# Kernel tuning notes

Measured on AMD Instinct MI355X. Metric: run time of the kernel, lower is better.

The kernel has to match this reference:

```python
import jax, jax.numpy as jnp
import numpy as np

B, T, C, HS = 32, 2048, 1024, 64

def setup_inputs() -> dict:
    key = jax.random.key(0)
    k1, k2, k3, k4 = jax.random.split(key, 4)
    x = jax.random.normal(k1, (B, T, C), dtype=jnp.float32)
    Wk = jax.random.normal(k2, (C, HS), dtype=jnp.float32) * (C ** -0.5)
    Wq = jax.random.normal(k3, (C, HS), dtype=jnp.float32) * (C ** -0.5)
    Wv = jax.random.normal(k4, (C, HS), dtype=jnp.float32) * (C ** -0.5)
    return {"x": x, "Wk": Wk, "Wq": Wq, "Wv": Wv}

def reference(x, Wk, Wq, Wv):
    # x: [B,T,C]; bias-free projections
    k = jnp.einsum('btc,ch->bth', x, Wk)   # [B,T,HS]
    q = jnp.einsum('btc,ch->bth', x, Wq)   # [B,T,HS]
    v = jnp.einsum('btc,ch->bth', x, Wv)   # [B,T,HS]
    Tdim = x.shape[1]
    Cdim = x.shape[2]
    scale = jax.lax.rsqrt(jnp.float32(Cdim))  # NOTE: source scales by rsqrt(C), not head_size
    wei = jnp.einsum('bth,bsh->bts', q, k) * scale  # [B,T,T]
    causal = jnp.tril(jnp.ones((Tdim, Tdim), dtype=bool))
    wei = jnp.where(causal, wei, -jnp.inf)
    wei = jax.nn.softmax(wei, axis=-1)
    out = jnp.einsum('bts,bsh->bth', wei, v)  # [B,T,HS]
    return out
```

## Files before the change

kernel.cpp:

```cpp
#include <hip/hip_runtime.h>
#include <hip/hip_bf16.h>

#define Bn 32
#define Tn 2048
#define Cn 1024
#define HSn 64

typedef __attribute__((ext_vector_type(8))) short short8;
typedef __attribute__((ext_vector_type(4))) float floatx4;

#if __has_builtin(__builtin_amdgcn_exp2f)
#define EXP2F __builtin_amdgcn_exp2f
#else
#define EXP2F exp2f
#endif

static __device__ __forceinline__ short f2bf(float f) {
    union { float f; unsigned u; } v; v.f = f;
    unsigned r = v.u + 0x7FFFu + ((v.u >> 16) & 1u);
    return (short)(r >> 16);
}
static __device__ __forceinline__ short f2bf_fast(float f) {
    union { float f; unsigned u; } v; v.f = f;
    return (short)((v.u + 0x8000u) >> 16);
}

static __device__ __forceinline__ void async16(const void* g, void* l) {
    __builtin_amdgcn_global_load_lds((const __attribute__((address_space(1))) void*)g,
                                     (__attribute__((address_space(3))) void*)l,
                                     16, 0, 0);
}

__global__ __launch_bounds__(256) void swz_w(const float* __restrict__ Wk,
                                             const float* __restrict__ Wq,
                                             const float* __restrict__ Wv,
                                             short* __restrict__ wswz) {
    int e = blockIdx.x * 256 + threadIdx.x;
    int j    = e & 7;
    int lane = (e >> 3) & 63;
    int grp  = e >> 9;
    int nt   = grp % 12;
    int kc   = grp / 12;
    int q = lane >> 4, m = lane & 15;
    int k = kc * 32 + q * 8 + j;
    int n = nt * 16 + m;
    const float* W = (n < 64) ? Wq : ((n < 128) ? Wk : Wv);
    wswz[e] = f2bf(W[k * 64 + (n & 63)]);
}

__global__ __launch_bounds__(256, 2) void qkv_gemm(const float* __restrict__ x,
                                                   const short* __restrict__ wswz,
                                                   short* __restrict__ qb,
                                                   short* __restrict__ kb,
                                                   short* __restrict__ vt) {
    __shared__ __align__(16) char lds[2][28 * 1024];

    int tid = threadIdx.x;
    int w = tid >> 6, l = tid & 63;
    int quad = l >> 4, m = l & 15;
    int r0 = blockIdx.x * 128;

    floatx4 acc[2][12];
#pragma unroll
    for (int r = 0; r < 2; r++)
#pragma unroll
        for (int nt = 0; nt < 12; nt++) acc[r][nt] = (floatx4)(0.0f);

    auto stage = [&](int kc, int bsel) {
        char* ab = &lds[bsel][0];
        char* bb = &lds[bsel][16 * 1024];
#pragma unroll
        for (int i = 0; i < 2; i++) {
            int rt = 2 * w + i;
            const float* src = x + (size_t)(r0 + rt * 16 + m) * Cn + kc * 32 + quad * 8;
            async16(src,     ab + rt * 2048 + l * 16);
            async16(src + 4, ab + rt * 2048 + 1024 + l * 16);
        }
#pragma unroll
        for (int i = 0; i < 3; i++) {
            int nt = 3 * w + i;
            const short* src = wswz + ((size_t)(kc * 12 + nt) * 64 + l) * 8;
            async16(src, bb + nt * 1024 + l * 16);
        }
    };

    stage(0, 0);
    for (int kc = 0; kc < 32; kc++) {
        __syncthreads();
        if (kc < 31) stage(kc + 1, (kc + 1) & 1);

        const char* ab = &lds[kc & 1][0];
        const char* bb = &lds[kc & 1][16 * 1024];

        short8 af[2];
#pragma unroll
        for (int r = 0; r < 2; r++) {
            int rt = 2 * w + r;
            float4 a0 = *(const float4*)(ab + rt * 2048 + l * 16);
            float4 a1 = *(const float4*)(ab + rt * 2048 + 1024 + l * 16);
            short8 t;
            t[0] = f2bf(a0.x); t[1] = f2bf(a0.y); t[2] = f2bf(a0.z); t[3] = f2bf(a0.w);
            t[4] = f2bf(a1.x); t[5] = f2bf(a1.y); t[6] = f2bf(a1.z); t[7] = f2bf(a1.w);
            af[r] = t;
        }
#pragma unroll
        for (int nt = 0; nt < 12; nt++) {
            short8 bf = *(const short8*)(bb + nt * 1024 + l * 16);
            acc[0][nt] = __builtin_amdgcn_mfma_f32_16x16x32_bf16(af[0], bf, acc[0][nt], 0, 0, 0);
            acc[1][nt] = __builtin_amdgcn_mfma_f32_16x16x32_bf16(af[1], bf, acc[1][nt], 0, 0, 0);
        }
    }

#pragma unroll
    for (int r = 0; r < 2; r++) {
        int rt = 2 * w + r;
#pragma unroll
        for (int reg = 0; reg < 4; reg++) {
            int g = r0 + rt * 16 + quad * 4 + reg;
            int b = g >> 11, t = g & (Tn - 1);
#pragma unroll
            for (int nt = 0; nt < 4; nt++)
                qb[(size_t)g * HSn + nt * 16 + m] = f2bf(acc[r][nt][reg]);
#pragma unroll
            for (int nt = 0; nt < 4; nt++)
                kb[(size_t)g * HSn + nt * 16 + m] = f2bf(acc[r][4 + nt][reg]);
#pragma unroll
            for (int nt = 0; nt < 4; nt++)
                vt[((size_t)b * HSn + nt * 16 + m) * Tn + t] = f2bf(acc[r][8 + nt][reg]);
        }
    }
}

__global__ __launch_bounds__(256, 4) void attn(const short* __restrict__ qb,
                                               const short* __restrict__ kb,
                                               const short* __restrict__ vt,
                                               float* __restrict__ out) {
    __shared__ __align__(16) short p_lds[4][16][72];
    __shared__ __align__(16) float comb[2][64][20];

    int tid = threadIdx.x;
    int w = tid >> 6, l = tid & 63;
    int quad = l >> 4, m = l & 15;
    int b  = blockIdx.x >> 5;
    int pb = blockIdx.x & 31;
    int pairSlot = w >> 1;
    int parity   = w & 1;
    int pairIdx  = pb * 2 + pairSlot;

    const short* kbbase = kb + (size_t)b * Tn * HSn;
    const short* vtbase = vt + (size_t)b * HSn * Tn;
    const float sl2e = 0.045084220027780106f;

    for (int half = 0; half < 2; half++) {
        int c = half ? (127 - pairIdx) : pairIdx;
        int r0 = c * 16;
        int jmax = c >> 2;

        size_t qoff = ((size_t)b * Tn + r0 + m) * HSn;
        short8 qf0 = *(const short8*)(qb + qoff + quad * 8);
        short8 qf1 = *(const short8*)(qb + qoff + 32 + quad * 8);

        floatx4 o[4];
#pragma unroll
        for (int i = 0; i < 4; i++) o[i] = (floatx4)(0.0f);
        float ps[4] = {0.f, 0.f, 0.f, 0.f};

        for (int j = parity; j <= jmax; j += 2) {
            floatx4 s[4];
#pragma unroll
            for (int i = 0; i < 4; i++) s[i] = (floatx4)(0.0f);
            const short* kt = kbbase + (size_t)j * 64 * HSn;
#pragma unroll
            for (int kc = 0; kc < 2; kc++) {
                short8 aq = kc ? qf1 : qf0;
#pragma unroll
                for (int nt = 0; nt < 4; nt++) {
                    short8 bk = *(const short8*)(kt + (size_t)(nt * 16 + m) * HSn + kc * 32 + quad * 8);
                    s[nt] = __builtin_amdgcn_mfma_f32_16x16x32_bf16(aq, bk, s[nt], 0, 0, 0);
                }
            }

            const short* vj = vtbase + j * 64;
            short8 bv[2][4];
#pragma unroll
            for (int kc = 0; kc < 2; kc++)
#pragma unroll
                for (int nt = 0; nt < 4; nt++)
                    bv[kc][nt] = *(const short8*)(vj + (size_t)(nt * 16 + m) * Tn + kc * 32 + quad * 8);

            if (j == jmax) {
                int rbase = r0 + quad * 4;
#pragma unroll
                for (int nt = 0; nt < 4; nt++)
#pragma unroll
                    for (int reg = 0; reg < 4; reg++) {
                        float p = EXP2F(s[nt][reg] * sl2e);
                        p = (j * 64 + nt * 16 + m > rbase + reg) ? 0.0f : p;
                        s[nt][reg] = p;
                        ps[reg] += p;
                    }
            } else {
#pragma unroll
                for (int nt = 0; nt < 4; nt++)
#pragma unroll
                    for (int reg = 0; reg < 4; reg++) {
                        float p = EXP2F(s[nt][reg] * sl2e);
                        s[nt][reg] = p;
                        ps[reg] += p;
                    }
            }

            asm volatile("" ::: "memory");
#pragma unroll
            for (int nt = 0; nt < 4; nt++)
#pragma unroll
                for (int reg = 0; reg < 4; reg++)
                    p_lds[w][quad * 4 + reg][nt * 16 + m] = f2bf_fast(s[nt][reg]);
            asm volatile("" ::: "memory");
            short8 ap0 = *(const short8*)(&p_lds[w][m][quad * 8]);
            short8 ap1 = *(const short8*)(&p_lds[w][m][32 + quad * 8]);

#pragma unroll
            for (int nt = 0; nt < 4; nt++)
                o[nt] = __builtin_amdgcn_mfma_f32_16x16x32_bf16(ap0, bv[0][nt], o[nt], 0, 0, 0);
#pragma unroll
            for (int nt = 0; nt < 4; nt++)
                o[nt] = __builtin_amdgcn_mfma_f32_16x16x32_bf16(ap1, bv[1][nt], o[nt], 0, 0, 0);
        }

        if (parity == 1) {
#pragma unroll
            for (int nt = 0; nt < 4; nt++)
                *(floatx4*)&comb[pairSlot][l][nt * 4] = o[nt];
            floatx4 pv; pv[0] = ps[0]; pv[1] = ps[1]; pv[2] = ps[2]; pv[3] = ps[3];
            *(floatx4*)&comb[pairSlot][l][16] = pv;
        }
        __syncthreads();
        if (parity == 0) {
#pragma unroll
            for (int nt = 0; nt < 4; nt++) {
                floatx4 t = *(const floatx4*)&comb[pairSlot][l][nt * 4];
                o[nt] += t;
            }
            floatx4 tp = *(const floatx4*)&comb[pairSlot][l][16];
            ps[0] += tp[0]; ps[1] += tp[1]; ps[2] += tp[2]; ps[3] += tp[3];
#pragma unroll
            for (int off = 1; off < 16; off <<= 1)
#pragma unroll
                for (int reg = 0; reg < 4; reg++)
                    ps[reg] += __shfl_xor(ps[reg], off, 64);
#pragma unroll
            for (int reg = 0; reg < 4; reg++) {
                float inv = 1.0f / ps[reg];
                int g = r0 + quad * 4 + reg;
#pragma unroll
                for (int nt = 0; nt < 4; nt++)
                    out[((size_t)b * Tn + g) * HSn + nt * 16 + m] = o[nt][reg] * inv;
            }
        }
        __syncthreads();
    }
}

extern "C" void kernel_launch(void* const* d_in, const int* in_sizes, int n_in,
                              void* d_out, int out_size, void* d_ws, size_t ws_size,
                              hipStream_t stream) {
    const float* x  = (const float*)d_in[0];
    const float* Wk = (const float*)d_in[1];
    const float* Wq = (const float*)d_in[2];
    const float* Wv = (const float*)d_in[3];
    float* out = (float*)d_out;

    char* ws = (char*)d_ws;
    short* wswz = (short*)ws;
    short* qb   = (short*)(ws + (1 << 19));
    short* kb   = (short*)(ws + (1 << 19) + (8 << 20));
    short* vt   = (short*)(ws + (1 << 19) + (16 << 20));

    swz_w<<<dim3(768), dim3(256), 0, stream>>>(Wk, Wq, Wv, wswz);
    qkv_gemm<<<dim3(512), dim3(256), 0, stream>>>(x, wswz, qb, kb, vt);
    attn<<<dim3(Bn * 32), dim3(256), 0, stream>>>(qb, kb, vt, out);
}
```

Before: 524.3 us.

## Stage K/V tiles in swizzled LDS shared by all four waves of attention block

The attention kernel now has each block handle one 64-row query tile per phase, with each wave owning 16 rows. K and V tiles are double-buffered into XOR-swizzled LDS with async copies, so the four waves share one load per tile instead of each reading from global memory. This drops the parity split and the LDS combine step, halves the grid to 512 blocks and lowers the occupancy hint to 2. The QKV GEMM staging pattern for x is also rearranged so each row's global reads are more contiguous. The risks are added barrier cost per tile and fewer blocks in flight.

New measurement: 449.8 us. -14.2%, faster.

```diff
diff --git a/kernel.cpp b/kernel.cpp
--- a/kernel.cpp
+++ b/kernel.cpp
@@ -69,12 +69,15 @@
     auto stage = [&](int kc, int bsel) {
         char* ab = &lds[bsel][0];
         char* bb = &lds[bsel][16 * 1024];
+        int srow = l & 15, sc = l >> 4;
 #pragma unroll
         for (int i = 0; i < 2; i++) {
             int rt = 2 * w + i;
-            const float* src = x + (size_t)(r0 + rt * 16 + m) * Cn + kc * 32 + quad * 8;
-            async16(src,     ab + rt * 2048 + l * 16);
-            async16(src + 4, ab + rt * 2048 + 1024 + l * 16);
+            const float* rbase = x + (size_t)(r0 + rt * 16 + srow) * Cn + kc * 32;
+#pragma unroll
+            for (int h = 0; h < 2; h++)
+                async16(rbase + h * 16 + sc * 4,
+                        ab + rt * 2048 + h * 1024 + l * 16);
         }
 #pragma unroll
         for (int i = 0; i < 3; i++) {
@@ -84,6 +87,8 @@
         }
     };
 
+    int c0 = (quad & 1) * 2, hh = quad >> 1;
+
     stage(0, 0);
     for (int kc = 0; kc < 32; kc++) {
         __syncthreads();
@@ -96,8 +101,9 @@
 #pragma unroll
         for (int r = 0; r < 2; r++) {
             int rt = 2 * w + r;
-            float4 a0 = *(const float4*)(ab + rt * 2048 + l * 16);
-            float4 a1 = *(const float4*)(ab + rt * 2048 + 1024 + l * 16);
+            const char* ap = ab + rt * 2048 + hh * 1024 + (c0 * 16 + m) * 16;
+            float4 a0 = *(const float4*)(ap);
+            float4 a1 = *(const float4*)(ap + 256);
             short8 t;
             t[0] = f2bf(a0.x); t[1] = f2bf(a0.y); t[2] = f2bf(a0.z); t[3] = f2bf(a0.w);
             t[4] = f2bf(a1.x); t[5] = f2bf(a1.y); t[6] = f2bf(a1.z); t[7] = f2bf(a1.w);
@@ -131,30 +137,41 @@
     }
 }
 
-__global__ __launch_bounds__(256, 4) void attn(const short* __restrict__ qb,
+__global__ __launch_bounds__(256, 2) void attn(const short* __restrict__ qb,
                                                const short* __restrict__ kb,
                                                const short* __restrict__ vt,
                                                float* __restrict__ out) {
+    __shared__ __align__(16) short kbuf[2][64 * 64];
+    __shared__ __align__(16) short vbuf[2][64 * 64];
     __shared__ __align__(16) short p_lds[4][16][72];
-    __shared__ __align__(16) float comb[2][64][20];
 
     int tid = threadIdx.x;
     int w = tid >> 6, l = tid & 63;
     int quad = l >> 4, m = l & 15;
-    int b  = blockIdx.x >> 5;
-    int pb = blockIdx.x & 31;
-    int pairSlot = w >> 1;
-    int parity   = w & 1;
-    int pairIdx  = pb * 2 + pairSlot;
+    int b = blockIdx.x >> 4;
+    int p = blockIdx.x & 15;
 
     const short* kbbase = kb + (size_t)b * Tn * HSn;
     const short* vtbase = vt + (size_t)b * HSn * Tn;
     const float sl2e = 0.045084220027780106f;
 
-    for (int half = 0; half < 2; half++) {
-        int c = half ? (127 - pairIdx) : pairIdx;
-        int r0 = c * 16;
-        int jmax = c >> 2;
+    int srow8 = l >> 3;
+    int schunk = l & 7;
+    auto stageKV = [&](int j, int s) {
+#pragma unroll
+        for (int i = 0; i < 2; i++) {
+            int r = w * 16 + i * 8 + srow8;
+            int c = schunk ^ (r & 7);
+            async16(kbbase + ((size_t)(j * 64 + r)) * HSn + c * 8,
+                    (char*)&kbuf[s][(w * 16 + i * 8) * 64] + l * 16);
+            async16(vtbase + (size_t)r * Tn + j * 64 + c * 8,
+                    (char*)&vbuf[s][(w * 16 + i * 8) * 64] + l * 16);
+        }
+    };
+
+    for (int phase = 0; phase < 2; phase++) {
+        int qt = phase ? (31 - p) : p;
+        int r0 = qt * 64 + w * 16;
 
         size_t qoff = ((size_t)b * Tn + r0 + m) * HSn;
         short8 qf0 = *(const short8*)(qb + qoff + quad * 8);
@@ -165,48 +182,48 @@
         for (int i = 0; i < 4; i++) o[i] = (floatx4)(0.0f);
         float ps[4] = {0.f, 0.f, 0.f, 0.f};
 
-        for (int j = parity; j <= jmax; j += 2) {
+        stageKV(0, 0);
+        for (int j = 0; j <= qt; j++) {
+            __syncthreads();
+            if (j < qt) stageKV(j + 1, (j + 1) & 1);
+
+            const short* kt = &kbuf[j & 1][0];
+            const short* vv = &vbuf[j & 1][0];
+            int swz = m & 7;
+
             floatx4 s[4];
 #pragma unroll
             for (int i = 0; i < 4; i++) s[i] = (floatx4)(0.0f);
-            const short* kt = kbbase + (size_t)j * 64 * HSn;
 #pragma unroll
             for (int kc = 0; kc < 2; kc++) {
                 short8 aq = kc ? qf1 : qf0;
 #pragma unroll
                 for (int nt = 0; nt < 4; nt++) {
-                    short8 bk = *(const short8*)(kt + (size_t)(nt * 16 + m) * HSn + kc * 32 + quad * 8);
+                    short8 bk = *(const short8*)(kt + (nt * 16 + m) * 64 +
+                                                 ((kc * 4 + quad) ^ swz) * 8);
                     s[nt] = __builtin_amdgcn_mfma_f32_16x16x32_bf16(aq, bk, s[nt], 0, 0, 0);
                 }
             }
 
-            const short* vj = vtbase + j * 64;
-            short8 bv[2][4];
-#pragma unroll
-            for (int kc = 0; kc < 2; kc++)
+            if (j == qt) {
+                int rloc = w * 16 + quad * 4;
 #pragma unroll
                 for (int nt = 0; nt < 4; nt++)
-                    bv[kc][nt] = *(const short8*)(vj + (size_t)(nt * 16 + m) * Tn + kc * 32 + quad * 8);
-
-            if (j == jmax) {
-                int rbase = r0 + quad * 4;
-#pragma unroll
-                for (int nt = 0; nt < 4; nt++)
 #pragma unroll
                     for (int reg = 0; reg < 4; reg++) {
-                        float p = EXP2F(s[nt][reg] * sl2e);
-                        p = (j * 64 + nt * 16 + m > rbase + reg) ? 0.0f : p;
-                        s[nt][reg] = p;
-                        ps[reg] += p;
+                        float pv = EXP2F(s[nt][reg] * sl2e);
+                        pv = (nt * 16 + m > rloc + reg) ? 0.0f : pv;
+                        s[nt][reg] = pv;
+                        ps[reg] += pv;
                     }
             } else {
 #pragma unroll
                 for (int nt = 0; nt < 4; nt++)
 #pragma unroll
                     for (int reg = 0; reg < 4; reg++) {
-                        float p = EXP2F(s[nt][reg] * sl2e);
-                        s[nt][reg] = p;
-                        ps[reg] += p;
+                        float pv = EXP2F(s[nt][reg] * sl2e);
+                        s[nt][reg] = pv;
+                        ps[reg] += pv;
                     }
             }
 
@@ -221,44 +238,31 @@
             short8 ap1 = *(const short8*)(&p_lds[w][m][32 + quad * 8]);
 
 #pragma unroll
-            for (int nt = 0; nt < 4; nt++)
-                o[nt] = __builtin_amdgcn_mfma_f32_16x16x32_bf16(ap0, bv[0][nt], o[nt], 0, 0, 0);
-#pragma unroll
-            for (int nt = 0; nt < 4; nt++)
-                o[nt] = __builtin_amdgcn_mfma_f32_16x16x32_bf16(ap1, bv[1][nt], o[nt], 0, 0, 0);
-        }
-
-        if (parity == 1) {
-#pragma unroll
-            for (int nt = 0; nt < 4; nt++)
-                *(floatx4*)&comb[pairSlot][l][nt * 4] = o[nt];
-            floatx4 pv; pv[0] = ps[0]; pv[1] = ps[1]; pv[2] = ps[2]; pv[3] = ps[3];
-            *(floatx4*)&comb[pairSlot][l][16] = pv;
+            for (int nt = 0; nt < 4; nt++) {
+                short8 bv0 = *(const short8*)(vv + (nt * 16 + m) * 64 + ((0 + quad) ^ swz) * 8);
+                o[nt] = __builtin_amdgcn_mfma_f32_16x16x32_bf16(ap0, bv0, o[nt], 0, 0, 0);
+            }
+#pragma unroll
+            for (int nt = 0; nt < 4; nt++) {
+                short8 bv1 = *(const short8*)(vv + (nt * 16 + m) * 64 + ((4 + quad) ^ swz) * 8);
+                o[nt] = __builtin_amdgcn_mfma_f32_16x16x32_bf16(ap1, bv1, o[nt], 0, 0, 0);
+            }
         }
         __syncthreads();
-        if (parity == 0) {
-#pragma unroll
-            for (int nt = 0; nt < 4; nt++) {
-                floatx4 t = *(const floatx4*)&comb[pairSlot][l][nt * 4];
-                o[nt] += t;
-            }
-            floatx4 tp = *(const floatx4*)&comb[pairSlot][l][16];
-            ps[0] += tp[0]; ps[1] += tp[1]; ps[2] += tp[2]; ps[3] += tp[3];
-#pragma unroll
-            for (int off = 1; off < 16; off <<= 1)
-#pragma unroll
-                for (int reg = 0; reg < 4; reg++)
-                    ps[reg] += __shfl_xor(ps[reg], off, 64);
-#pragma unroll
-            for (int reg = 0; reg < 4; reg++) {
-                float inv = 1.0f / ps[reg];
-                int g = r0 + quad * 4 + reg;
-#pragma unroll
-                for (int nt = 0; nt < 4; nt++)
-                    out[((size_t)b * Tn + g) * HSn + nt * 16 + m] = o[nt][reg] * inv;
-            }
-        }
-        __syncthreads();
+
+#pragma unroll
+        for (int off = 1; off < 16; off <<= 1)
+#pragma unroll
+            for (int reg = 0; reg < 4; reg++)
+                ps[reg] += __shfl_xor(ps[reg], off, 64);
+#pragma unroll
+        for (int reg = 0; reg < 4; reg++) {
+            float inv = 1.0f / ps[reg];
+            int g = r0 + quad * 4 + reg;
+#pragma unroll
+            for (int nt = 0; nt < 4; nt++)
+                out[((size_t)b * Tn + g) * HSn + nt * 16 + m] = o[nt][reg] * inv;
+        }
     }
 }
 
@@ -279,5 +283,5 @@
 
     swz_w<<<dim3(768), dim3(256), 0, stream>>>(Wk, Wq, Wv, wswz);
     qkv_gemm<<<dim3(512), dim3(256), 0, stream>>>(x, wswz, qb, kb, vt);
-    attn<<<dim3(Bn * 32), dim3(256), 0, stream>>>(qb, kb, vt, out);
-}
+    attn<<<dim3(512), dim3(256), 0, stream>>>(qb, kb, vt, out);
+}
```
